# Performance work log

Hardware: AMD Instinct MI355X
Metric: run time of the kernel (lower is better)

## Reference

```python
import jax, jax.numpy as jnp
import numpy as np

K = 16

def _local_cov(points):
    # points: [B, N, 3]. FoldingNet-style local covariance feature.
    xx = jnp.sum(points * points, axis=-1)                       # [B,N]
    inner = jnp.einsum('bnd,bmd->bnm', points, points)           # [B,N,N]
    pd = -xx[:, :, None] + 2.0 * inner - xx[:, None, :]          # negative sq dist
    _, idx = jax.lax.top_k(pd, K)                                # [B,N,K] nearest first (self at 0)
    n0 = jnp.take_along_axis(points, idx[:, :, 0][:, :, None], axis=1)  # [B,N,3]
    n1 = jnp.take_along_axis(points, idx[:, :, 1][:, :, None], axis=1)  # [B,N,3]
    cov = n0[..., :, None] * n1[..., None, :]                    # [B,N,3,3] outer product
    B, N = points.shape[0], points.shape[1]
    return jnp.concatenate([points, cov.reshape(B, N, 9)], axis=-1)     # [B,N,12]

def _stage(x, w1, b1, wr, br, w2, b2):
    h = jax.nn.relu(x @ w1 + b1)
    h = jax.nn.relu(h + (h @ wr + br))   # ResidualLinearLayer then ReLU
    return h @ w2 + b2                   # [B,N,1]

def setup_inputs() -> dict:
    key = jax.random.key(0)
    ks = jax.random.split(key, 16)
    B, N, F = 8, 4096, 512
    s = 0.02
    d = {
        'latent': jax.random.normal(ks[0], (B, N, F), jnp.float32),
        'reconstructed_points': jax.random.normal(ks[1], (B, 3, N), jnp.float32),
        's1_w1': jax.random.normal(ks[2], (F + 12, F), jnp.float32) * s,
        's1_b1': jnp.zeros((F,), jnp.float32),
        's1_wr': jax.random.normal(ks[3], (F, F), jnp.float32) * s,
        's1_br': jnp.zeros((F,), jnp.float32),
        's1_w2': jax.random.normal(ks[4], (F, 1), jnp.float32) * s,
        's1_b2': jnp.zeros((1,), jnp.float32),
        's2_w1': jax.random.normal(ks[5], (F + 1, F), jnp.float32) * s,
        's2_b1': jnp.zeros((F,), jnp.float32),
        's2_wr': jax.random.normal(ks[6], (F, F), jnp.float32) * s,
        's2_br': jnp.zeros((F,), jnp.float32),
        's2_w2': jax.random.normal(ks[7], (F, 1), jnp.float32) * s,
        's2_b2': jnp.zeros((1,), jnp.float32),
        's3_w1': jax.random.normal(ks[8], (F + 1, F), jnp.float32) * s,
        's3_b1': jnp.zeros((F,), jnp.float32),
        's3_wr': jax.random.normal(ks[9], (F, F), jnp.float32) * s,
        's3_br': jnp.zeros((F,), jnp.float32),
        's3_w2': jax.random.normal(ks[10], (F, 1), jnp.float32) * s,
        's3_b2': jnp.zeros((1,), jnp.float32),
    }
    return d

def reference(latent, reconstructed_points,
              s1_w1, s1_b1, s1_wr, s1_br, s1_w2, s1_b2,
              s2_w1, s2_b1, s2_wr, s2_br, s2_w2, s2_b2,
              s3_w1, s3_b1, s3_wr, s3_br, s3_w2, s3_b2):
    pts = jnp.transpose(reconstructed_points, (0, 2, 1))   # [B,N,3]
    local = _local_cov(pts)                                 # [B,N,12]
    f1 = jnp.concatenate([latent, local], axis=-1)
    std1 = _stage(f1, s1_w1, s1_b1, s1_wr, s1_br, s1_w2, s1_b2)
    f2 = jnp.concatenate([latent, std1], axis=-1)
    std2 = std1 + _stage(f2, s2_w1, s2_b1, s2_wr, s2_br, s2_w2, s2_b2)
    f3 = jnp.concatenate([latent, std2], axis=-1)
    std3 = std2 + _stage(f3, s3_w1, s3_b1, s3_wr, s3_br, s3_w2, s3_b2)
    return std3   # [B,N,1]
```

## Files before the change

### kernel.cpp

```cpp
#include <hip/hip_runtime.h>

typedef __bf16 bf16x8 __attribute__((ext_vector_type(8)));
typedef float f32x16 __attribute__((ext_vector_type(16)));

__device__ __forceinline__ unsigned short f2bf(float f) {
  unsigned u = __float_as_uint(f);
  u += 0x7FFFu + ((u >> 16) & 1u);
  return (unsigned short)(u >> 16);
}

__device__ __forceinline__ void gload_lds16(const void* g, void* l) {
  __builtin_amdgcn_global_load_lds((const __attribute__((address_space(1))) void*)g,
                                   (__attribute__((address_space(3))) void*)l,
                                   16, 0, 0);
}

#define NPTS 4096
#define LDX 576

__global__ __launch_bounds__(256) void convw6_kernel(
    const float* w0, const float* w1, const float* w2,
    const float* r0, const float* r1, const float* r2,
    unsigned short* d0, unsigned short* d1, unsigned short* d2,
    unsigned short* e0, unsigned short* e1, unsigned short* e2) {
  int z = blockIdx.z;
  const float* src; unsigned short* dst; int Ksrc, Kpad, addI;
  switch (z) {
    case 0: src = w0; dst = d0; Ksrc = 524; Kpad = 576; addI = 0; break;
    case 1: src = w1; dst = d1; Ksrc = 513; Kpad = 576; addI = 0; break;
    case 2: src = w2; dst = d2; Ksrc = 513; Kpad = 576; addI = 0; break;
    case 3: src = r0; dst = e0; Ksrc = 512; Kpad = 512; addI = 1; break;
    case 4: src = r1; dst = e1; Ksrc = 512; Kpad = 512; addI = 1; break;
    default: src = r2; dst = e2; Ksrc = 512; Kpad = 512; addI = 1; break;
  }
  int k0 = blockIdx.x * 32;
  if (k0 >= Kpad) return;
  __shared__ float tile[32][33];
  int n0 = blockIdx.y * 32;
  int tx = threadIdx.x & 31, ty = threadIdx.x >> 5;
#pragma unroll
  for (int r = 0; r < 32; r += 8) {
    int k = k0 + ty + r, n = n0 + tx;
    tile[ty + r][tx] = (k < Ksrc) ? src[(size_t)k * 512 + n] : 0.f;
  }
  __syncthreads();
#pragma unroll
  for (int r = 0; r < 32; r += 8) {
    int n = n0 + ty + r, k = k0 + tx;
    float v = tile[tx][ty + r];
    if (addI && n == k) v += 1.0f;
    dst[(size_t)n * Kpad + k] = f2bf(v);
  }
}

__global__ __launch_bounds__(256) void conv_latent_kernel(const float* __restrict__ latent,
                                                          unsigned short* __restrict__ X) {
  size_t idx = (size_t)blockIdx.x * 256 + threadIdx.x;
  size_t m = idx >> 7;
  int c4 = (int)(idx & 127) * 4;
  float4 v = *(const float4*)(latent + m * 512 + c4);
  ushort4 o;
  o.x = f2bf(v.x); o.y = f2bf(v.y); o.z = f2bf(v.z); o.w = f2bf(v.w);
  *(ushort4*)(X + m * LDX + c4) = o;
}

__device__ __forceinline__ void merge1(float& v, int& j, int mk) {
  float ov = __shfl_xor(v, mk); int oj = __shfl_xor(j, mk);
  bool take = (ov > v) || (ov == v && oj < j);
  v = take ? ov : v; j = take ? oj : j;
}

__global__ __launch_bounds__(512) void knn_kernel(const float* __restrict__ rp,
                                                  unsigned short* __restrict__ X) {
  __shared__ float4 P[NPTS];
  int b = blockIdx.y;
  const float* base = rp + (size_t)b * 3 * NPTS;
  for (int j = threadIdx.x; j < NPTS; j += 512) {
    float x = base[j], y = base[NPTS + j], z = base[2 * NPTS + j];
    float xx = __fadd_rn(__fadd_rn(__fmul_rn(x, x), __fmul_rn(y, y)), __fmul_rn(z, z));
    P[j] = make_float4(x, y, z, -xx);
  }
  __syncthreads();
  int wave = threadIdx.x >> 6, lane = threadIdx.x & 63;
  int grp = lane >> 4, slice = lane & 15;
  int il0 = wave * 8 + grp * 2;
  int ia = blockIdx.x * 64 + il0;
  int ib = ia + 1;
  float4 pa = P[ia], pb = P[ib];
  float ax = 2.f * pa.x, ay = 2.f * pa.y, az = 2.f * pa.z;
  float bx = 2.f * pb.x, by = 2.f * pb.y, bz = 2.f * pb.z;
  float va = -3.4e38f, vb = -3.4e38f;
  int ta = 0, tb = 0;
  int sta = ((ia & 15) == slice) ? (ia >> 4) : -1;
  int stb = ((ib & 15) == slice) ? (ib >> 4) : -1;
  const float4* pp = P + slice;
#pragma unroll 8
  for (int t = 0; t < NPTS / 16; ++t) {
    float4 pj = pp[t * 16];
    float ea = __builtin_fmaf(ax, pj.x, __builtin_fmaf(ay, pj.y,
               __builtin_fmaf(az, pj.z, pj.w)));
    float eb = __builtin_fmaf(bx, pj.x, __builtin_fmaf(by, pj.y,
               __builtin_fmaf(bz, pj.z, pj.w)));
    ea = (t == sta) ? -3.4e38f : ea;
    eb = (t == stb) ? -3.4e38f : eb;
    bool ca = ea > va; va = ca ? ea : va; ta = ca ? t : ta;
    bool cb = eb > vb; vb = cb ? eb : vb; tb = cb ? t : tb;
  }
  int ja = ta * 16 + slice, jb = tb * 16 + slice;
#pragma unroll
  for (int mk = 1; mk <= 8; mk <<= 1) {
    merge1(va, ja, mk);
    merge1(vb, jb, mk);
  }
  if (slice == 0) {
#pragma unroll
    for (int p = 0; p < 2; ++p) {
      float4 pi = (p == 0) ? pa : pb;
      float4 p1 = P[(p == 0) ? ja : jb];
      size_t row = (size_t)b * NPTS + ia + p;
      unsigned short* xp = X + row * LDX + 512;
      float vals[12] = { pi.x, pi.y, pi.z,
                         pi.x * p1.x, pi.x * p1.y, pi.x * p1.z,
                         pi.y * p1.x, pi.y * p1.y, pi.y * p1.z,
                         pi.z * p1.x, pi.z * p1.y, pi.z * p1.z };
#pragma unroll
      for (int k = 0; k < 12; ++k) xp[k] = f2bf(vals[k]);
#pragma unroll
      for (int k = 12; k < 32; ++k) xp[k] = 0;
    }
  }
}

#define BM 256
#define BN 128
#define BK 64
#define GRP 520

__global__ __launch_bounds__(512) void gemm_relu_kernel(
    const unsigned short* __restrict__ Xb, const unsigned short* __restrict__ Wt,
    const float* __restrict__ bias, unsigned short* __restrict__ H,
    int K, int ldx, int ldw) {
  __shared__ unsigned short As[32 * GRP];
  __shared__ unsigned short Bs[16 * GRP];
  const int t = threadIdx.x;
  const int wave = t >> 6, lane = t & 63;
  const int m0 = blockIdx.y * BM, n0 = blockIdx.x * BN;
  const int wm = (wave >> 1) * 64, wn = (wave & 1) * 64;
  const int srow = lane >> 3;
  const int sslot = (lane & 7) ^ srow;
  const int l31 = lane & 31, hi = lane >> 5;
  const int w7 = l31 & 7, g2 = l31 >> 3;
  f32x16 acc[2][2] = {};
  for (int kt = 0; kt < K; kt += BK) {
#pragma unroll
    for (int r = 0; r < 4; ++r) {
      int ga = wave + r * 8;
      gload_lds16(Xb + (size_t)(m0 + ga * 8 + srow) * ldx + kt + sslot * 8, As + ga * GRP);
    }
#pragma unroll
    for (int r = 0; r < 2; ++r) {
      int gb = wave + r * 8;
      gload_lds16(Wt + (size_t)(n0 + gb * 8 + srow) * ldw + kt + sslot * 8, Bs + gb * GRP);
    }
    __syncthreads();
#pragma unroll
    for (int ks = 0; ks < 4; ++ks) {
      int qx = (ks * 2 + hi) ^ w7;
      bf16x8 a[2], bb[2];
#pragma unroll
      for (int i = 0; i < 2; ++i)
        a[i] = *(const bf16x8*)(As + ((wm >> 3) + i * 4 + g2) * GRP + w7 * 64 + qx * 8);
#pragma unroll
      for (int j = 0; j < 2; ++j)
        bb[j] = *(const bf16x8*)(Bs + ((wn >> 3) + j * 4 + g2) * GRP + w7 * 64 + qx * 8);
#pragma unroll
      for (int i = 0; i < 2; ++i)
#pragma unroll
        for (int j = 0; j < 2; ++j)
          acc[i][j] = __builtin_amdgcn_mfma_f32_32x32x16_bf16(a[i], bb[j], acc[i][j], 0, 0, 0);
    }
    __syncthreads();
  }
#pragma unroll
  for (int j = 0; j < 2; ++j) {
    int col = n0 + wn + j * 32 + l31;
    float bv = bias[col];
#pragma unroll
    for (int i = 0; i < 2; ++i) {
#pragma unroll
      for (int rg = 0; rg < 16; ++rg) {
        int row = m0 + wm + i * 32 + (rg & 3) + 8 * (rg >> 2) + 4 * hi;
        float v = acc[i][j][rg] + bv;
        v = v > 0.f ? v : 0.f;
        H[(size_t)row * 512 + col] = f2bf(v);
      }
    }
  }
}

__global__ __launch_bounds__(512) void gemm_res_kernel(
    const unsigned short* __restrict__ H1, const unsigned short* __restrict__ Wt,
    const float* __restrict__ br, const float* __restrict__ w2,
    float* __restrict__ so) {
  __shared__ unsigned short As[32 * GRP];
  __shared__ unsigned short Bs[16 * GRP];
  const int t = threadIdx.x;
  const int wave = t >> 6, lane = t & 63;
  const int m0 = blockIdx.y * BM, n0 = blockIdx.x * BN;
  const int wm = (wave >> 1) * 64, wn = (wave & 1) * 64;
  const int srow = lane >> 3;
  const int sslot = (lane & 7) ^ srow;
  const int l31 = lane & 31, hi = lane >> 5;
  const int w7 = l31 & 7, g2 = l31 >> 3;
  f32x16 acc[2][2] = {};
  for (int kt = 0; kt < 512; kt += BK) {
#pragma unroll
    for (int r = 0; r < 4; ++r) {
      int ga = wave + r * 8;
      gload_lds16(H1 + (size_t)(m0 + ga * 8 + srow) * 512 + kt + sslot * 8, As + ga * GRP);
    }
#pragma unroll
    for (int r = 0; r < 2; ++r) {
      int gb = wave + r * 8;
      gload_lds16(Wt + (size_t)(n0 + gb * 8 + srow) * 512 + kt + sslot * 8, Bs + gb * GRP);
    }
    __syncthreads();
#pragma unroll
    for (int ks = 0; ks < 4; ++ks) {
      int qx = (ks * 2 + hi) ^ w7;
      bf16x8 a[2], bb[2];
#pragma unroll
      for (int i = 0; i < 2; ++i)
        a[i] = *(const bf16x8*)(As + ((wm >> 3) + i * 4 + g2) * GRP + w7 * 64 + qx * 8);
#pragma unroll
      for (int j = 0; j < 2; ++j)
        bb[j] = *(const bf16x8*)(Bs + ((wn >> 3) + j * 4 + g2) * GRP + w7 * 64 + qx * 8);
#pragma unroll
      for (int i = 0; i < 2; ++i)
#pragma unroll
        for (int j = 0; j < 2; ++j)
          acc[i][j] = __builtin_amdgcn_mfma_f32_32x32x16_bf16(a[i], bb[j], acc[i][j], 0, 0, 0);
    }
    __syncthreads();
  }
  float pr[2][16];
#pragma unroll
  for (int i = 0; i < 2; ++i)
#pragma unroll
    for (int rg = 0; rg < 16; ++rg) pr[i][rg] = 0.f;
#pragma unroll
  for (int j = 0; j < 2; ++j) {
    int col = n0 + wn + j * 32 + l31;
    float bv = br[col], wv = w2[col];
#pragma unroll
    for (int i = 0; i < 2; ++i)
#pragma unroll
      for (int rg = 0; rg < 16; ++rg) {
        float v = acc[i][j][rg] + bv;
        v = v > 0.f ? v : 0.f;
        pr[i][rg] += v * wv;
      }
  }
#pragma unroll
  for (int i = 0; i < 2; ++i)
#pragma unroll
    for (int rg = 0; rg < 16; ++rg) {
      float s = pr[i][rg];
      s += __shfl_xor(s, 1); s += __shfl_xor(s, 2); s += __shfl_xor(s, 4);
      s += __shfl_xor(s, 8); s += __shfl_xor(s, 16);
      if (l31 == 0) {
        int row = m0 + wm + i * 32 + (rg & 3) + 8 * (rg >> 2) + 4 * hi;
        atomicAdd(&so[row], s);
      }
    }
}

__global__ __launch_bounds__(256) void init_so_kernel(float* so, const float* b2) {
  int m = blockIdx.x * 256 + threadIdx.x;
  so[m] = b2[0];
}
__global__ __launch_bounds__(256) void update_kernel(float* std_cum, float* so,
                                                     unsigned short* X,
                                                     const float* b2_next, int first) {
  int m = blockIdx.x * 256 + threadIdx.x;
  float s = so[m];
  if (!first) s += std_cum[m];
  std_cum[m] = s;
  unsigned short* xp = X + (size_t)m * LDX + 512;
  xp[0] = f2bf(s);
#pragma unroll
  for (int k = 1; k < 12; ++k) xp[k] = 0;
  so[m] = b2_next[0];
}
__global__ __launch_bounds__(256) void finalize_kernel(float* out, const float* std_cum,
                                                       const float* so) {
  int m = blockIdx.x * 256 + threadIdx.x;
  out[m] = std_cum[m] + so[m];
}

extern "C" void kernel_launch(void* const* d_in, const int* in_sizes, int n_in,
                              void* d_out, int out_size, void* d_ws, size_t ws_size,
                              hipStream_t stream) {
  const int B = 8, N = NPTS, M = B * N;
  const float* latent = (const float*)d_in[0];
  const float* rp = (const float*)d_in[1];
  const float* w1[3] = {(const float*)d_in[2], (const float*)d_in[8], (const float*)d_in[14]};
  const float* b1[3] = {(const float*)d_in[3], (const float*)d_in[9], (const float*)d_in[15]};
  const float* wr[3] = {(const float*)d_in[4], (const float*)d_in[10], (const float*)d_in[16]};
  const float* br[3] = {(const float*)d_in[5], (const float*)d_in[11], (const float*)d_in[17]};
  const float* w2[3] = {(const float*)d_in[6], (const float*)d_in[12], (const float*)d_in[18]};
  const float* b2[3] = {(const float*)d_in[7], (const float*)d_in[13], (const float*)d_in[19]};

  char* ws = (char*)d_ws;
  auto carve = [&](size_t bytes) {
    char* p = ws;
    ws += (bytes + 255) & ~(size_t)255;
    return p;
  };
  unsigned short* X  = (unsigned short*)carve((size_t)M * LDX * 2);
  unsigned short* H1 = (unsigned short*)carve((size_t)M * 512 * 2);
  unsigned short* W1t[3], *Wrt[3];
  for (int s = 0; s < 3; ++s) W1t[s] = (unsigned short*)carve((size_t)512 * LDX * 2);
  for (int s = 0; s < 3; ++s) Wrt[s] = (unsigned short*)carve((size_t)512 * 512 * 2);
  float* std_cum = (float*)carve((size_t)M * 4);
  float* so      = (float*)carve((size_t)M * 4);

  convw6_kernel<<<dim3(LDX / 32, 16, 6), 256, 0, stream>>>(
      w1[0], w1[1], w1[2], wr[0], wr[1], wr[2],
      W1t[0], W1t[1], W1t[2], Wrt[0], Wrt[1], Wrt[2]);
  conv_latent_kernel<<<(M * 128) / 256, 256, 0, stream>>>(latent, X);
  knn_kernel<<<dim3(N / 64, B), 512, 0, stream>>>(rp, X);
  init_so_kernel<<<M / 256, 256, 0, stream>>>(so, b2[0]);

  for (int s = 0; s < 3; ++s) {
    gemm_relu_kernel<<<dim3(BN / 128 * 4, M / BM), 512, 0, stream>>>(X, W1t[s], b1[s], H1,
                                                                     LDX, LDX, LDX);
    gemm_res_kernel<<<dim3(4, M / BM), 512, 0, stream>>>(H1, Wrt[s], br[s], w2[s], so);
    if (s < 2)
      update_kernel<<<M / 256, 256, 0, stream>>>(std_cum, so, X, b2[s + 1], s == 0 ? 1 : 0);
  }
  finalize_kernel<<<M / 256, 256, 0, stream>>>((float*)d_out, std_cum, so);
}
```

Before: 351.8 us.

## Prepack weights into MFMA fragment layout, load B from global, double-buffer A

Weights are rewritten in the conversion kernel into a fragment-packed layout so each lane can load its B operand for the MFMA directly from global memory, removing the B tile from LDS. The A tile is double-buffered in dynamically sized LDS with prefetch of the next K step, which cuts one barrier per iteration and overlaps loading with compute. In exchange, B loads hit global memory or L2 on every iteration and each wave reads its own copy, which may add latency if the loads are not hidden.

```diff
diff --git a/kernel.cpp b/kernel.cpp
--- a/kernel.cpp
+++ b/kernel.cpp
@@ -44,12 +44,15 @@
     tile[ty + r][tx] = (k < Ksrc) ? src[(size_t)k * 512 + n] : 0.f;
   }
   __syncthreads();
+  int KB = Kpad >> 4;
 #pragma unroll
   for (int r = 0; r < 32; r += 8) {
     int n = n0 + ty + r, k = k0 + tx;
     float v = tile[tx][ty + r];
     if (addI && n == k) v += 1.0f;
-    dst[(size_t)n * Kpad + k] = f2bf(v);
+    int nb = n >> 5, kb = k >> 4;
+    int ln = (n & 31) + ((k >> 3) & 1) * 32;
+    dst[((size_t)nb * KB + kb) * 512 + ln * 8 + (k & 7)] = f2bf(v);
   }
 }
 
@@ -137,11 +140,10 @@
 #define GRP 520
 
 __global__ __launch_bounds__(512) void gemm_relu_kernel(
-    const unsigned short* __restrict__ Xb, const unsigned short* __restrict__ Wt,
+    const unsigned short* __restrict__ Xb, const unsigned short* __restrict__ Wp,
     const float* __restrict__ bias, unsigned short* __restrict__ H,
-    int K, int ldx, int ldw) {
-  __shared__ unsigned short As[32 * GRP];
-  __shared__ unsigned short Bs[16 * GRP];
+    int K, int ldx) {
+  extern __shared__ unsigned short As[];
   const int t = threadIdx.x;
   const int wave = t >> 6, lane = t & 63;
   const int m0 = blockIdx.y * BM, n0 = blockIdx.x * BN;
@@ -150,36 +152,48 @@
   const int sslot = (lane & 7) ^ srow;
   const int l31 = lane & 31, hi = lane >> 5;
   const int w7 = l31 & 7, g2 = l31 >> 3;
+  const int KB = K >> 4;
+  const unsigned short* bb0 = Wp + ((size_t)((n0 + wn) >> 5)) * KB * 512 + lane * 8;
+  const unsigned short* bb1 = bb0 + (size_t)KB * 512;
   f32x16 acc[2][2] = {};
-  for (int kt = 0; kt < K; kt += BK) {
-#pragma unroll
-    for (int r = 0; r < 4; ++r) {
-      int ga = wave + r * 8;
-      gload_lds16(Xb + (size_t)(m0 + ga * 8 + srow) * ldx + kt + sslot * 8, As + ga * GRP);
-    }
-#pragma unroll
-    for (int r = 0; r < 2; ++r) {
-      int gb = wave + r * 8;
-      gload_lds16(Wt + (size_t)(n0 + gb * 8 + srow) * ldw + kt + sslot * 8, Bs + gb * GRP);
-    }
+  const int NK = K / BK;
+#pragma unroll
+  for (int r = 0; r < 4; ++r) {
+    int ga = wave + r * 8;
+    gload_lds16(Xb + (size_t)(m0 + ga * 8 + srow) * ldx + sslot * 8, As + ga * GRP);
+  }
+  for (int kt = 0; kt < NK; ++kt) {
+    const int p = kt & 1;
+    unsigned short* cur = (unsigned short*)As + p * (32 * GRP);
+    unsigned short* nxt = (unsigned short*)As + (p ^ 1) * (32 * GRP);
     __syncthreads();
+    if (kt + 1 < NK) {
+#pragma unroll
+      for (int r = 0; r < 4; ++r) {
+        int ga = wave + r * 8;
+        gload_lds16(Xb + (size_t)(m0 + ga * 8 + srow) * ldx + (kt + 1) * BK + sslot * 8,
+                    nxt + ga * GRP);
+      }
+    }
+    bf16x8 bfr[2][4];
+#pragma unroll
+    for (int ks = 0; ks < 4; ++ks) {
+      bfr[0][ks] = *(const bf16x8*)(bb0 + (size_t)(kt * 4 + ks) * 512);
+      bfr[1][ks] = *(const bf16x8*)(bb1 + (size_t)(kt * 4 + ks) * 512);
+    }
 #pragma unroll
     for (int ks = 0; ks < 4; ++ks) {
       int qx = (ks * 2 + hi) ^ w7;
-      bf16x8 a[2], bb[2];
+      bf16x8 a[2];
 #pragma unroll
       for (int i = 0; i < 2; ++i)
-        a[i] = *(const bf16x8*)(As + ((wm >> 3) + i * 4 + g2) * GRP + w7 * 64 + qx * 8);
-#pragma unroll
-      for (int j = 0; j < 2; ++j)
-        bb[j] = *(const bf16x8*)(Bs + ((wn >> 3) + j * 4 + g2) * GRP + w7 * 64 + qx * 8);
+        a[i] = *(const bf16x8*)(cur + ((wm >> 3) + i * 4 + g2) * GRP + w7 * 64 + qx * 8);
 #pragma unroll
       for (int i = 0; i < 2; ++i)
 #pragma unroll
         for (int j = 0; j < 2; ++j)
-          acc[i][j] = __builtin_amdgcn_mfma_f32_32x32x16_bf16(a[i], bb[j], acc[i][j], 0, 0, 0);
-    }
-    __syncthreads();
+          acc[i][j] = __builtin_amdgcn_mfma_f32_32x32x16_bf16(a[i], bfr[j][ks], acc[i][j], 0, 0, 0);
+    }
   }
 #pragma unroll
   for (int j = 0; j < 2; ++j) {
@@ -199,11 +213,10 @@
 }
 
 __global__ __launch_bounds__(512) void gemm_res_kernel(
-    const unsigned short* __restrict__ H1, const unsigned short* __restrict__ Wt,
+    const unsigned short* __restrict__ H1, const unsigned short* __restrict__ Wp,
     const float* __restrict__ br, const float* __restrict__ w2,
     float* __restrict__ so) {
-  __shared__ unsigned short As[32 * GRP];
-  __shared__ unsigned short Bs[16 * GRP];
+  extern __shared__ unsigned short As[];
   const int t = threadIdx.x;
   const int wave = t >> 6, lane = t & 63;
   const int m0 = blockIdx.y * BM, n0 = blockIdx.x * BN;
@@ -212,36 +225,47 @@
   const int sslot = (lane & 7) ^ srow;
   const int l31 = lane & 31, hi = lane >> 5;
   const int w7 = l31 & 7, g2 = l31 >> 3;
+  const int KB = 32;
+  const unsigned short* bb0 = Wp + ((size_t)((n0 + wn) >> 5)) * KB * 512 + lane * 8;
+  const unsigned short* bb1 = bb0 + (size_t)KB * 512;
   f32x16 acc[2][2] = {};
-  for (int kt = 0; kt < 512; kt += BK) {
-#pragma unroll
-    for (int r = 0; r < 4; ++r) {
-      int ga = wave + r * 8;
-      gload_lds16(H1 + (size_t)(m0 + ga * 8 + srow) * 512 + kt + sslot * 8, As + ga * GRP);
-    }
-#pragma unroll
-    for (int r = 0; r < 2; ++r) {
-      int gb = wave + r * 8;
-      gload_lds16(Wt + (size_t)(n0 + gb * 8 + srow) * 512 + kt + sslot * 8, Bs + gb * GRP);
-    }
+#pragma unroll
+  for (int r = 0; r < 4; ++r) {
+    int ga = wave + r * 8;
+    gload_lds16(H1 + (size_t)(m0 + ga * 8 + srow) * 512 + sslot * 8, As + ga * GRP);
+  }
+  for (int kt = 0; kt < 8; ++kt) {
+    const int p = kt & 1;
+    unsigned short* cur = (unsigned short*)As + p * (32 * GRP);
+    unsigned short* nxt = (unsigned short*)As + (p ^ 1) * (32 * GRP);
     __syncthreads();
+    if (kt + 1 < 8) {
+#pragma unroll
+      for (int r = 0; r < 4; ++r) {
+        int ga = wave + r * 8;
+        gload_lds16(H1 + (size_t)(m0 + ga * 8 + srow) * 512 + (kt + 1) * BK + sslot * 8,
+                    nxt + ga * GRP);
+      }
+    }
+    bf16x8 bfr[2][4];
+#pragma unroll
+    for (int ks = 0; ks < 4; ++ks) {
+      bfr[0][ks] = *(const bf16x8*)(bb0 + (size_t)(kt * 4 + ks) * 512);
+      bfr[1][ks] = *(const bf16x8*)(bb1 + (size_t)(kt * 4 + ks) * 512);
+    }
 #pragma unroll
     for (int ks = 0; ks < 4; ++ks) {
       int qx = (ks * 2 + hi) ^ w7;
-      bf16x8 a[2], bb[2];
+      bf16x8 a[2];
 #pragma unroll
       for (int i = 0; i < 2; ++i)
-        a[i] = *(const bf16x8*)(As + ((wm >> 3) + i * 4 + g2) * GRP + w7 * 64 + qx * 8);
-#pragma unroll
-      for (int j = 0; j < 2; ++j)
-        bb[j] = *(const bf16x8*)(Bs + ((wn >> 3) + j * 4 + g2) * GRP + w7 * 64 + qx * 8);
+        a[i] = *(const bf16x8*)(cur + ((wm >> 3) + i * 4 + g2) * GRP + w7 * 64 + qx * 8);
 #pragma unroll
       for (int i = 0; i < 2; ++i)
 #pragma unroll
         for (int j = 0; j < 2; ++j)
-          acc[i][j] = __builtin_amdgcn_mfma_f32_32x32x16_bf16(a[i], bb[j], acc[i][j], 0, 0, 0);
-    }
-    __syncthreads();
+          acc[i][j] = __builtin_amdgcn_mfma_f32_32x32x16_bf16(a[i], bfr[j][ks], acc[i][j], 0, 0, 0);
+    }
   }
   float pr[2][16];
 #pragma unroll
@@ -332,10 +356,11 @@
   knn_kernel<<<dim3(N / 64, B), 512, 0, stream>>>(rp, X);
   init_so_kernel<<<M / 256, 256, 0, stream>>>(so, b2[0]);
 
+  const size_t lds_bytes = 2 * 32 * GRP * sizeof(unsigned short);
   for (int s = 0; s < 3; ++s) {
-    gemm_relu_kernel<<<dim3(BN / 128 * 4, M / BM), 512, 0, stream>>>(X, W1t[s], b1[s], H1,
-                                                                     LDX, LDX, LDX);
-    gemm_res_kernel<<<dim3(4, M / BM), 512, 0, stream>>>(H1, Wrt[s], br[s], w2[s], so);
+    gemm_relu_kernel<<<dim3(4, M / BM), 512, lds_bytes, stream>>>(X, W1t[s], b1[s], H1,
+                                                                  LDX, LDX);
+    gemm_res_kernel<<<dim3(4, M / BM), 512, lds_bytes, stream>>>(H1, Wrt[s], br[s], w2[s], so);
     if (s < 2)
       update_kernel<<<M / 256, 256, 0, stream>>>(std_cum, so, X, b2[s + 1], s == 0 ? 1 : 0);
   }
```

After: 376.7 us. +7.1%, slower.
